# Performance work log

Hardware: AMD Instinct MI355X
Metric: run time of the kernel (lower is better)

The kernel has to match this reference:

```python
import jax, jax.numpy as jnp
import numpy as np

IN_DIM, OUT_DIM = 4096, 11008
NUM_SUBDIM, KS = 1376, 256
DS = OUT_DIM // NUM_SUBDIM  # 8
BATCH = 32


def setup_inputs() -> dict:
    key = jax.random.key(0)
    k1, k2, k3, k4 = jax.random.split(key, 4)
    x = jax.random.normal(k1, (BATCH, IN_DIM), dtype=jnp.float32)
    vectors = jax.random.normal(k2, (NUM_SUBDIM, KS, DS), dtype=jnp.float32)
    bias = jax.random.normal(k3, (OUT_DIM,), dtype=jnp.float32)
    indexes = jax.random.randint(k4, (IN_DIM, NUM_SUBDIM), 0, KS, dtype=jnp.int64)
    return {"x": x, "vectors": vectors, "bias": bias, "indexes": indexes}


def reference(x, vectors, bias, indexes):
    in_dim, num_subdim = indexes.shape
    ds = vectors.shape[-1]
    # PQ dequant: gather codewords per (row, subspace) -> [in_dim, num_subdim, Ds]
    # vectors[d, indexes[i, d]] via broadcast of arange(num_subdim) against indexes.
    dims = jnp.arange(num_subdim)
    weight = vectors[dims, indexes].reshape(in_dim, num_subdim * ds)  # [in_dim, out_dim]
    return x @ weight + bias
```

## Files before the change

### kernel.cpp

```cpp
#include <hip/hip_runtime.h>

#define IN_DIM  4096
#define OUT_DIM 11008
#define NSUB    1376
#define KSQ     256
#define DSUB    8
#define BATCH   32

#define DTILE   16
#define NTILE   128
#define KC      128
#define KSPLIT  16
#define KPB     (IN_DIM / KSPLIT)
#define NCHUNK  (KPB / KC)
#define NBLK    (OUT_DIM / NTILE)

typedef unsigned short ushort_t;
typedef unsigned int   uint_t;
typedef __attribute__((ext_vector_type(8))) short bf16x8;
typedef __attribute__((ext_vector_type(4))) float f32x4;

#define SW_STRIDE 136
#define SX_STRIDE 136
#define SI_STRIDE 132

#define VEC_N   (NSUB * KSQ * DSUB)
#define XBF_OFF 5636096
#define PREP_V  (VEC_N / 2)
#define PREP_X  (BATCH * IN_DIM / 2)
#define PREP_O  (BATCH * OUT_DIM)
#define PREP_N  (PREP_V + PREP_X + PREP_O)

__device__ __forceinline__ ushort_t f2bf(float f) {
    union { float f; uint_t u; } a; a.f = f;
    uint_t u = a.u;
    u += 0x7fffu + ((u >> 16) & 1u);
    return (ushort_t)(u >> 16);
}

__global__ __launch_bounds__(256) void pq_prep(
    const float* __restrict__ x, const float* __restrict__ vecs,
    const float* __restrict__ bias,
    uint_t* __restrict__ vbf, uint_t* __restrict__ xbf, float* __restrict__ out)
{
    int tid = blockIdx.x * 256 + threadIdx.x;
    if (tid < PREP_V) {
        float2 v = ((const float2*)vecs)[tid];
        vbf[tid] = (uint_t)f2bf(v.x) | ((uint_t)f2bf(v.y) << 16);
    } else if (tid < PREP_V + PREP_X) {
        int i = tid - PREP_V;
        float2 v = ((const float2*)x)[i];
        xbf[i] = (uint_t)f2bf(v.x) | ((uint_t)f2bf(v.y) << 16);
    } else {
        int i = tid - (PREP_V + PREP_X);
        out[i] = bias[i % OUT_DIM];
    }
}

__global__ __launch_bounds__(256) void pq_main(
    const ushort_t* __restrict__ xbf, const uint4* __restrict__ vbf,
    const int* __restrict__ idx, float* __restrict__ out)
{
    __shared__ ushort_t sW[NTILE * SW_STRIDE];
    __shared__ ushort_t sX[BATCH * SX_STRIDE];
    __shared__ int      sI[DTILE * SI_STRIDE];

    const int t    = threadIdx.x;
    const int nblk = blockIdx.x;
    const int kblk = blockIdx.y;
    const int d0   = nblk * DTILE;
    const int kbase = kblk * KPB;

    const int wave = t >> 6;
    const int lane = t & 63;
    const int l15  = lane & 15;
    const int l4   = lane >> 4;

    const int gd = t >> 4;
    const int go = t & 15;

    f32x4 acc[2][2];
    #pragma unroll
    for (int i = 0; i < 2; ++i)
        #pragma unroll
        for (int j = 0; j < 2; ++j)
            acc[i][j] = (f32x4)0.0f;

    int   ireg[8];
    uint4 xreg[2];

    {
        const int i0 = kbase;
        #pragma unroll
        for (int p = 0; p < 8; ++p) {
            int f = p * 256 + t, ii = f >> 4, dd = f & 15;
            ireg[p] = idx[(size_t)(i0 + ii) * NSUB + (d0 + dd)];
        }
        #pragma unroll
        for (int p = 0; p < 2; ++p) {
            int f = p * 256 + t, b = f >> 4, q = f & 15;
            xreg[p] = ((const uint4*)xbf)[b * (IN_DIM / 8) + i0 / 8 + q];
        }
    }

    for (int c = 0; c < NCHUNK; ++c) {
        __syncthreads();

        #pragma unroll
        for (int p = 0; p < 8; ++p) {
            int f = p * 256 + t, ii = f >> 4, dd = f & 15;
            sI[dd * SI_STRIDE + ii] = ireg[p];
        }
        #pragma unroll
        for (int p = 0; p < 2; ++p) {
            int f = p * 256 + t, b = f >> 4, q = f & 15;
            *(uint4*)&sX[b * SX_STRIDE + q * 8] = xreg[p];
        }
        __syncthreads();

        int kk[8];
        #pragma unroll
        for (int s = 0; s < 8; ++s)
            kk[s] = sI[gd * SI_STRIDE + go * 8 + s];

        uint4 q[8];
        #pragma unroll
        for (int s = 0; s < 8; ++s)
            q[s] = vbf[(d0 + gd) * KSQ + kk[s]];

        if (c + 1 < NCHUNK) {
            const int i0n = kbase + (c + 1) * KC;
            #pragma unroll
            for (int p = 0; p < 8; ++p) {
                int f = p * 256 + t, ii = f >> 4, dd = f & 15;
                ireg[p] = idx[(size_t)(i0n + ii) * NSUB + (d0 + dd)];
            }
            #pragma unroll
            for (int p = 0; p < 2; ++p) {
                int f = p * 256 + t, b = f >> 4, qq = f & 15;
                xreg[p] = ((const uint4*)xbf)[b * (IN_DIM / 8) + i0n / 8 + qq];
            }
        }

        #pragma unroll
        for (int j = 0; j < 8; ++j) {
            const uint_t sel = (j & 1) ? 0x07060302u : 0x05040100u;
            uint_t c0 = (j >> 1) == 0 ? q[0].x : (j >> 1) == 1 ? q[0].y : (j >> 1) == 2 ? q[0].z : q[0].w;
            uint_t c1 = (j >> 1) == 0 ? q[1].x : (j >> 1) == 1 ? q[1].y : (j >> 1) == 2 ? q[1].z : q[1].w;
            uint_t c2 = (j >> 1) == 0 ? q[2].x : (j >> 1) == 1 ? q[2].y : (j >> 1) == 2 ? q[2].z : q[2].w;
            uint_t c3 = (j >> 1) == 0 ? q[3].x : (j >> 1) == 1 ? q[3].y : (j >> 1) == 2 ? q[3].z : q[3].w;
            uint_t c4 = (j >> 1) == 0 ? q[4].x : (j >> 1) == 1 ? q[4].y : (j >> 1) == 2 ? q[4].z : q[4].w;
            uint_t c5 = (j >> 1) == 0 ? q[5].x : (j >> 1) == 1 ? q[5].y : (j >> 1) == 2 ? q[5].z : q[5].w;
            uint_t c6 = (j >> 1) == 0 ? q[6].x : (j >> 1) == 1 ? q[6].y : (j >> 1) == 2 ? q[6].z : q[6].w;
            uint_t c7 = (j >> 1) == 0 ? q[7].x : (j >> 1) == 1 ? q[7].y : (j >> 1) == 2 ? q[7].z : q[7].w;
            uint4 wv;
            wv.x = __builtin_amdgcn_perm(c1, c0, sel);
            wv.y = __builtin_amdgcn_perm(c3, c2, sel);
            wv.z = __builtin_amdgcn_perm(c5, c4, sel);
            wv.w = __builtin_amdgcn_perm(c7, c6, sel);
            *(uint4*)&sW[(gd * 8 + j) * SW_STRIDE + go * 8] = wv;
        }
        __syncthreads();

        #pragma unroll
        for (int kq = 0; kq < KC / 32; ++kq) {
            bf16x8 A[2], B[2];
            #pragma unroll
            for (int mt = 0; mt < 2; ++mt)
                A[mt] = *(const bf16x8*)
                    &sX[(mt * 16 + l15) * SX_STRIDE + kq * 32 + l4 * 8];
            #pragma unroll
            for (int nt = 0; nt < 2; ++nt)
                B[nt] = *(const bf16x8*)
                    &sW[(wave * 32 + nt * 16 + l15) * SW_STRIDE + kq * 32 + l4 * 8];
            #pragma unroll
            for (int mt = 0; mt < 2; ++mt)
                #pragma unroll
                for (int nt = 0; nt < 2; ++nt)
                    acc[mt][nt] = __builtin_amdgcn_mfma_f32_16x16x32_bf16(
                        A[mt], B[nt], acc[mt][nt], 0, 0, 0);
        }
    }

    #pragma unroll
    for (int mt = 0; mt < 2; ++mt)
        #pragma unroll
        for (int nt = 0; nt < 2; ++nt)
            #pragma unroll
            for (int r = 0; r < 4; ++r) {
                int row = mt * 16 + l4 * 4 + r;
                int col = nblk * NTILE + wave * 32 + nt * 16 + l15;
                atomicAdd(&out[(size_t)row * OUT_DIM + col], acc[mt][nt][r]);
            }
}

extern "C" void kernel_launch(void* const* d_in, const int* in_sizes, int n_in,
                              void* d_out, int out_size, void* d_ws, size_t ws_size,
                              hipStream_t stream) {
    const float* x    = (const float*)d_in[0];
    const float* vecs = (const float*)d_in[1];
    const float* bias = (const float*)d_in[2];
    const int*   idx  = (const int*)d_in[3];
    float* out = (float*)d_out;

    uint_t* vbf = (uint_t*)d_ws;
    uint_t* xbf = (uint_t*)((char*)d_ws + XBF_OFF);

    pq_prep<<<PREP_N / 256, 256, 0, stream>>>(x, vecs, bias, vbf, xbf, out);
    dim3 grid(NBLK, KSPLIT);
    pq_main<<<grid, 256, 0, stream>>>((const ushort_t*)xbf, (const uint4*)vbf,
                                      idx, out);
}
```

Before: 113.6 us.

## Restructure PQ GEMM with byte index transpose, LDS codebook, slab reduction

Adds a pre-pass that converts the int64-as-int index matrix into a transposed uint8 layout, which cuts index traffic in the main kernel. The main kernel now caches each subspace's 256 codewords in LDS, keeps x fragments in registers, and builds weight tiles per wave with XOR-swizzled LDS writes, with no block-wide barriers inside the loop. Tiles shrink to 64 columns so the grid has more blocks. Float atomics are replaced by per-split partial slabs plus a separate reduce kernel that also adds the bias. The cost is two extra launches and additional workspace traffic for the transposed indices and partial slabs.

```diff
diff --git a/kernel.cpp b/kernel.cpp
--- a/kernel.cpp
+++ b/kernel.cpp
@@ -7,9 +7,9 @@
 #define DSUB    8
 #define BATCH   32
 
-#define DTILE   16
-#define NTILE   128
-#define KC      128
+#define DTILE   8
+#define NTILE   64
+#define KC      64
 #define KSPLIT  16
 #define KPB     (IN_DIM / KSPLIT)
 #define NCHUNK  (KPB / KC)
@@ -17,19 +17,17 @@
 
 typedef unsigned short ushort_t;
 typedef unsigned int   uint_t;
+typedef unsigned char  uchar_t;
 typedef __attribute__((ext_vector_type(8))) short bf16x8;
 typedef __attribute__((ext_vector_type(4))) float f32x4;
 
-#define SW_STRIDE 136
-#define SX_STRIDE 136
-#define SI_STRIDE 132
-
-#define VEC_N   (NSUB * KSQ * DSUB)
-#define XBF_OFF 5636096
-#define PREP_V  (VEC_N / 2)
-#define PREP_X  (BATCH * IN_DIM / 2)
-#define PREP_O  (BATCH * OUT_DIM)
-#define PREP_N  (PREP_V + PREP_X + PREP_O)
+#define VEC_N    (NSUB * KSQ * DSUB)
+#define XBF_OFF  (VEC_N * 2)
+#define IDXT_OFF (XBF_OFF + BATCH * IN_DIM * 2)
+#define SLAB_OFF (IDXT_OFF + NSUB * IN_DIM)
+#define PREP_V   (VEC_N / 2)
+#define PREP_X   (BATCH * IN_DIM / 2)
+#define PREP_N   (PREP_V + PREP_X)
 
 __device__ __forceinline__ ushort_t f2bf(float f) {
     union { float f; uint_t u; } a; a.f = f;
@@ -40,158 +38,128 @@
 
 __global__ __launch_bounds__(256) void pq_prep(
     const float* __restrict__ x, const float* __restrict__ vecs,
-    const float* __restrict__ bias,
-    uint_t* __restrict__ vbf, uint_t* __restrict__ xbf, float* __restrict__ out)
+    uint_t* __restrict__ vbf, uint_t* __restrict__ xbf)
 {
     int tid = blockIdx.x * 256 + threadIdx.x;
     if (tid < PREP_V) {
         float2 v = ((const float2*)vecs)[tid];
         vbf[tid] = (uint_t)f2bf(v.x) | ((uint_t)f2bf(v.y) << 16);
-    } else if (tid < PREP_V + PREP_X) {
+    } else {
         int i = tid - PREP_V;
         float2 v = ((const float2*)x)[i];
         xbf[i] = (uint_t)f2bf(v.x) | ((uint_t)f2bf(v.y) << 16);
-    } else {
-        int i = tid - (PREP_V + PREP_X);
-        out[i] = bias[i % OUT_DIM];
     }
 }
 
-__global__ __launch_bounds__(256) void pq_main(
-    const ushort_t* __restrict__ xbf, const uint4* __restrict__ vbf,
-    const int* __restrict__ idx, float* __restrict__ out)
+__global__ __launch_bounds__(256) void pq_idxT(
+    const int* __restrict__ idx, uchar_t* __restrict__ idx8T)
 {
-    __shared__ ushort_t sW[NTILE * SW_STRIDE];
-    __shared__ ushort_t sX[BATCH * SX_STRIDE];
-    __shared__ int      sI[DTILE * SI_STRIDE];
+    __shared__ uchar_t sT[32][144];
+    const int k0 = blockIdx.x * 128, d0 = blockIdx.y * 32, t = threadIdx.x;
+    #pragma unroll
+    for (int p = 0; p < 16; ++p) {
+        int f = p * 256 + t;
+        int kk = f >> 5, dd = f & 31;
+        sT[dd][kk] = (uchar_t)idx[(size_t)(k0 + kk) * NSUB + d0 + dd];
+    }
+    __syncthreads();
+    int dd = t >> 3, seg = t & 7;
+    uint4 v = *(const uint4*)&sT[dd][seg * 16];
+    *(uint4*)&idx8T[(size_t)(d0 + dd) * IN_DIM + k0 + seg * 16] = v;
+}
+
+__global__ __launch_bounds__(256, 4) void pq_main(
+    const ushort_t* __restrict__ xbf, const uint4* __restrict__ vbf4,
+    const uchar_t* __restrict__ idx8T, float* __restrict__ slab)
+{
+    __shared__ uint4  sV4[4 * 512];
+    __shared__ uint_t sW32[4 * 16 * 32];
 
     const int t    = threadIdx.x;
+    const int w    = t >> 6;
+    const int lane = t & 63;
     const int nblk = blockIdx.x;
     const int kblk = blockIdx.y;
     const int d0   = nblk * DTILE;
     const int kbase = kblk * KPB;
 
-    const int wave = t >> 6;
-    const int lane = t & 63;
-    const int l15  = lane & 15;
-    const int l4   = lane >> 4;
-
-    const int gd = t >> 4;
-    const int go = t & 15;
-
-    f32x4 acc[2][2];
-    #pragma unroll
-    for (int i = 0; i < 2; ++i)
-        #pragma unroll
-        for (int j = 0; j < 2; ++j)
-            acc[i][j] = (f32x4)0.0f;
-
-    int   ireg[8];
-    uint4 xreg[2];
+    const int l15 = lane & 15;
+    const int l4  = lane >> 4;
+    const int dl  = lane >> 5;
+    const int q   = lane & 31;
 
     {
-        const int i0 = kbase;
+        const size_t src0 = (size_t)(d0 + w * 2) * KSQ;
         #pragma unroll
-        for (int p = 0; p < 8; ++p) {
-            int f = p * 256 + t, ii = f >> 4, dd = f & 15;
-            ireg[p] = idx[(size_t)(i0 + ii) * NSUB + (d0 + dd)];
-        }
-        #pragma unroll
-        for (int p = 0; p < 2; ++p) {
-            int f = p * 256 + t, b = f >> 4, q = f & 15;
-            xreg[p] = ((const uint4*)xbf)[b * (IN_DIM / 8) + i0 / 8 + q];
-        }
+        for (int p = 0; p < 8; ++p)
+            sV4[w * 512 + p * 64 + lane] = vbf4[src0 + p * 64 + lane];
     }
 
+    bf16x8 A[2][8];
+    #pragma unroll
+    for (int mt = 0; mt < 2; ++mt)
+        #pragma unroll
+        for (int kk = 0; kk < 8; ++kk)
+            A[mt][kk] = *(const bf16x8*)
+                &xbf[(size_t)(mt * 16 + l15) * IN_DIM + kbase + kk * 32 + l4 * 8];
+
+    f32x4 acc[2];
+    acc[0] = (f32x4)0.0f; acc[1] = (f32x4)0.0f;
+
+    const uchar_t* idxrow = idx8T + (size_t)(d0 + w * 2 + dl) * IN_DIM + kbase;
+    const int vbase = w * 512 + dl * 256;
+    const int Rbase = (w * 16 + dl * 8) * 32;
+
+    #pragma unroll
     for (int c = 0; c < NCHUNK; ++c) {
-        __syncthreads();
-
-        #pragma unroll
-        for (int p = 0; p < 8; ++p) {
-            int f = p * 256 + t, ii = f >> 4, dd = f & 15;
-            sI[dd * SI_STRIDE + ii] = ireg[p];
-        }
-        #pragma unroll
-        for (int p = 0; p < 2; ++p) {
-            int f = p * 256 + t, b = f >> 4, q = f & 15;
-            *(uint4*)&sX[b * SX_STRIDE + q * 8] = xreg[p];
-        }
-        __syncthreads();
-
-        int kk[8];
-        #pragma unroll
-        for (int s = 0; s < 8; ++s)
-            kk[s] = sI[gd * SI_STRIDE + go * 8 + s];
-
-        uint4 q[8];
-        #pragma unroll
-        for (int s = 0; s < 8; ++s)
-            q[s] = vbf[(d0 + gd) * KSQ + kk[s]];
-
-        if (c + 1 < NCHUNK) {
-            const int i0n = kbase + (c + 1) * KC;
-            #pragma unroll
-            for (int p = 0; p < 8; ++p) {
-                int f = p * 256 + t, ii = f >> 4, dd = f & 15;
-                ireg[p] = idx[(size_t)(i0n + ii) * NSUB + (d0 + dd)];
-            }
-            #pragma unroll
-            for (int p = 0; p < 2; ++p) {
-                int f = p * 256 + t, b = f >> 4, qq = f & 15;
-                xreg[p] = ((const uint4*)xbf)[b * (IN_DIM / 8) + i0n / 8 + qq];
-            }
-        }
+        uint_t bb = *(const ushort_t*)&idxrow[c * KC + q * 2];
+        uint4 g0 = sV4[vbase + (bb & 255)];
+        uint4 g1 = sV4[vbase + (bb >> 8)];
 
         #pragma unroll
         for (int j = 0; j < 8; ++j) {
             const uint_t sel = (j & 1) ? 0x07060302u : 0x05040100u;
-            uint_t c0 = (j >> 1) == 0 ? q[0].x : (j >> 1) == 1 ? q[0].y : (j >> 1) == 2 ? q[0].z : q[0].w;
-            uint_t c1 = (j >> 1) == 0 ? q[1].x : (j >> 1) == 1 ? q[1].y : (j >> 1) == 2 ? q[1].z : q[1].w;
-            uint_t c2 = (j >> 1) == 0 ? q[2].x : (j >> 1) == 1 ? q[2].y : (j >> 1) == 2 ? q[2].z : q[2].w;
-            uint_t c3 = (j >> 1) == 0 ? q[3].x : (j >> 1) == 1 ? q[3].y : (j >> 1) == 2 ? q[3].z : q[3].w;
-            uint_t c4 = (j >> 1) == 0 ? q[4].x : (j >> 1) == 1 ? q[4].y : (j >> 1) == 2 ? q[4].z : q[4].w;
-            uint_t c5 = (j >> 1) == 0 ? q[5].x : (j >> 1) == 1 ? q[5].y : (j >> 1) == 2 ? q[5].z : q[5].w;
-            uint_t c6 = (j >> 1) == 0 ? q[6].x : (j >> 1) == 1 ? q[6].y : (j >> 1) == 2 ? q[6].z : q[6].w;
-            uint_t c7 = (j >> 1) == 0 ? q[7].x : (j >> 1) == 1 ? q[7].y : (j >> 1) == 2 ? q[7].z : q[7].w;
-            uint4 wv;
-            wv.x = __builtin_amdgcn_perm(c1, c0, sel);
-            wv.y = __builtin_amdgcn_perm(c3, c2, sel);
-            wv.z = __builtin_amdgcn_perm(c5, c4, sel);
-            wv.w = __builtin_amdgcn_perm(c7, c6, sel);
-            *(uint4*)&sW[(gd * 8 + j) * SW_STRIDE + go * 8] = wv;
+            uint_t a0 = (j >> 1) == 0 ? g0.x : (j >> 1) == 1 ? g0.y : (j >> 1) == 2 ? g0.z : g0.w;
+            uint_t a1 = (j >> 1) == 0 ? g1.x : (j >> 1) == 1 ? g1.y : (j >> 1) == 2 ? g1.z : g1.w;
+            uint_t wv = __builtin_amdgcn_perm(a1, a0, sel);
+            int dw = ((((q >> 2) ^ j) << 2) | (q & 3));
+            sW32[Rbase + j * 32 + dw] = wv;
         }
-        __syncthreads();
 
         #pragma unroll
-        for (int kq = 0; kq < KC / 32; ++kq) {
-            bf16x8 A[2], B[2];
+        for (int kq = 0; kq < 2; ++kq) {
+            int u16 = (kq * 4 + l4) ^ (l15 & 7);
+            bf16x8 B = *(const bf16x8*)
+                ((const char*)sW32 + (w * 16 + l15) * 128 + u16 * 16);
             #pragma unroll
             for (int mt = 0; mt < 2; ++mt)
-                A[mt] = *(const bf16x8*)
-                    &sX[(mt * 16 + l15) * SX_STRIDE + kq * 32 + l4 * 8];
-            #pragma unroll
-            for (int nt = 0; nt < 2; ++nt)
-                B[nt] = *(const bf16x8*)
-                    &sW[(wave * 32 + nt * 16 + l15) * SW_STRIDE + kq * 32 + l4 * 8];
-            #pragma unroll
-            for (int mt = 0; mt < 2; ++mt)
-                #pragma unroll
-                for (int nt = 0; nt < 2; ++nt)
-                    acc[mt][nt] = __builtin_amdgcn_mfma_f32_16x16x32_bf16(
-                        A[mt], B[nt], acc[mt][nt], 0, 0, 0);
+                acc[mt] = __builtin_amdgcn_mfma_f32_16x16x32_bf16(
+                    A[mt][c * 2 + kq], B, acc[mt], 0, 0, 0);
         }
     }
 
+    float* sl = slab + (size_t)kblk * BATCH * OUT_DIM;
+    const int col = nblk * NTILE + w * 16 + l15;
     #pragma unroll
     for (int mt = 0; mt < 2; ++mt)
         #pragma unroll
-        for (int nt = 0; nt < 2; ++nt)
-            #pragma unroll
-            for (int r = 0; r < 4; ++r) {
-                int row = mt * 16 + l4 * 4 + r;
-                int col = nblk * NTILE + wave * 32 + nt * 16 + l15;
-                atomicAdd(&out[(size_t)row * OUT_DIM + col], acc[mt][nt][r]);
-            }
+        for (int r = 0; r < 4; ++r)
+            sl[(size_t)(mt * 16 + l4 * 4 + r) * OUT_DIM + col] = acc[mt][r];
+}
+
+__global__ __launch_bounds__(256) void pq_reduce(
+    const float* __restrict__ slab, const float* __restrict__ bias,
+    float* __restrict__ out)
+{
+    int i = blockIdx.x * 256 + threadIdx.x;
+    int m = i / (OUT_DIM / 4), n4 = i % (OUT_DIM / 4);
+    float4 s = ((const float4*)bias)[n4];
+    #pragma unroll
+    for (int kb = 0; kb < KSPLIT; ++kb) {
+        float4 v = ((const float4*)slab)[(size_t)(kb * BATCH + m) * (OUT_DIM / 4) + n4];
+        s.x += v.x; s.y += v.y; s.z += v.z; s.w += v.w;
+    }
+    ((float4*)out)[(size_t)m * (OUT_DIM / 4) + n4] = s;
 }
 
 extern "C" void kernel_launch(void* const* d_in, const int* in_sizes, int n_in,
@@ -203,11 +171,14 @@
     const int*   idx  = (const int*)d_in[3];
     float* out = (float*)d_out;
 
-    uint_t* vbf = (uint_t*)d_ws;
-    uint_t* xbf = (uint_t*)((char*)d_ws + XBF_OFF);
+    uint_t*  vbf   = (uint_t*)d_ws;
+    uint_t*  xbf   = (uint_t*)((char*)d_ws + XBF_OFF);
+    uchar_t* idx8T = (uchar_t*)((char*)d_ws + IDXT_OFF);
+    float*   slab  = (float*)((char*)d_ws + SLAB_OFF);
 
-    pq_prep<<<PREP_N / 256, 256, 0, stream>>>(x, vecs, bias, vbf, xbf, out);
-    dim3 grid(NBLK, KSPLIT);
-    pq_main<<<grid, 256, 0, stream>>>((const ushort_t*)xbf, (const uint4*)vbf,
-                                      idx, out);
+    pq_prep<<<PREP_N / 256, 256, 0, stream>>>(x, vecs, vbf, xbf);
+    pq_idxT<<<dim3(IN_DIM / 128, NSUB / 32), 256, 0, stream>>>(idx, idx8T);
+    pq_main<<<dim3(NBLK, KSPLIT), 256, 0, stream>>>(
+        (const ushort_t*)xbf, (const uint4*)vbf, idx8T, slab);
+    pq_reduce<<<(BATCH * OUT_DIM / 4) / 256, 256, 0, stream>>>(slab, bias, out);
 }
```

After: 116.1 us. 1.02x slower.
